# Performance work log

Hardware: AMD Instinct MI355X
Metric: run time of the kernel (lower is better)

The kernel has to match this reference:

```python
import jax, jax.numpy as jnp
import numpy as np

B = 8192      # batch
LAT = 256     # latent_dimension
HID = 512     # hidden_size
INP = 128     # input_size (n_layer_types + 1 feature)
T = 64        # max_length
MLP = 512     # fixed MLP width in source


def _lin(key, fan_in, fan_out):
    kw, kb = jax.random.split(key)
    s = 1.0 / np.sqrt(fan_in)
    W = jax.random.uniform(kw, (fan_in, fan_out), jnp.float32, -s, s)
    b = jax.random.uniform(kb, (fan_out,), jnp.float32, -s, s)
    return W, b


def setup_inputs() -> dict:
    key = jax.random.key(0)
    ks = jax.random.split(key, 16)
    x = jax.random.normal(ks[0], (B, LAT), jnp.float32)
    W1, b1 = _lin(ks[1], LAT, MLP)
    W2, b2 = _lin(ks[2], MLP, MLP)
    W3, b3 = _lin(ks[3], MLP, MLP)
    Wh1, bh1 = _lin(ks[4], MLP, MLP)
    Wh2, bh2 = _lin(ks[5], MLP, HID)
    Wc1, bc1 = _lin(ks[6], MLP, MLP)
    Wc2, bc2 = _lin(ks[7], MLP, HID)
    Wx1, bx1 = _lin(ks[8], MLP, MLP)
    Wx2, bx2 = _lin(ks[9], MLP, INP)
    Wih, bih = _lin(ks[10], INP, 4 * HID)   # LSTM input->gates (i,f,g,o)
    Whh, bhh = _lin(ks[11], HID, 4 * HID)   # LSTM hidden->gates
    Wp, bp = _lin(ks[12], HID, INP)          # predictor head
    return dict(x=x, W1=W1, b1=b1, W2=W2, b2=b2, W3=W3, b3=b3,
                Wh1=Wh1, bh1=bh1, Wh2=Wh2, bh2=bh2,
                Wc1=Wc1, bc1=bc1, Wc2=Wc2, bc2=bc2,
                Wx1=Wx1, bx1=bx1, Wx2=Wx2, bx2=bx2,
                Wih=Wih, bih=bih, Whh=Whh, bhh=bhh, Wp=Wp, bp=bp)


def _lrelu(v):
    return jnp.where(v >= 0, v, 0.2 * v)


def _head(v):
    # split [d-1, 1]: softmax over layer types, sigmoid on feature scalar
    lt = jax.nn.softmax(v[..., :-1], axis=-1)
    ft = jax.nn.sigmoid(v[..., -1:])
    return jnp.concatenate([lt, ft], axis=-1)


def reference(x, W1, b1, W2, b2, W3, b3, Wh1, bh1, Wh2, bh2,
              Wc1, bc1, Wc2, bc2, Wx1, bx1, Wx2, bx2,
              Wih, bih, Whh, bhh, Wp, bp):
    z = _lrelu(x @ W1 + b1)
    z = _lrelu(z @ W2 + b2)
    z = _lrelu(z @ W3 + b3)
    h = _lrelu(z @ Wh1 + bh1) @ Wh2 + bh2          # [B, HID]
    c = _lrelu(z @ Wc1 + bc1) @ Wc2 + bc2          # [B, HID]
    x0 = _head(_lrelu(z @ Wx1 + bx1) @ Wx2 + bx2)  # [B, INP]

    def step(carry, _):
        xt, h, c = carry
        g = xt @ Wih + h @ Whh + (bih + bhh)        # [B, 4*HID]
        i, f, gg, o = jnp.split(g, 4, axis=-1)      # torch gate order i,f,g,o
        c2 = jax.nn.sigmoid(f) * c + jax.nn.sigmoid(i) * jnp.tanh(gg)
        h2 = jax.nn.sigmoid(o) * jnp.tanh(c2)
        nxt = _head(h2 @ Wp + bp)
        return (nxt, h2, c2), nxt

    # The torch loop reruns the LSTM over the growing prefix with the same
    # initial (h,c) and takes the last output; by LSTM causality this equals
    _, ys = jax.lax.scan(step, (x0, h, c), None, length=T)
    return jnp.transpose(ys, (1, 0, 2))  # [B, T, INP]
```

## Files before the change

### kernel.cpp

```cpp
#include <hip/hip_runtime.h>


typedef _Float16 h16;
typedef __attribute__((ext_vector_type(8))) _Float16 f16x8;
typedef __attribute__((ext_vector_type(4))) float f32x4;

#define BB 8192
#define TT 64

__device__ __forceinline__ void gload16(const void* g, void* lds) {
  __builtin_amdgcn_global_load_lds(
      (const __attribute__((address_space(1))) unsigned int*)g,
      (__attribute__((address_space(3))) unsigned int*)lds, 16, 0, 0);
}

__device__ __forceinline__ float sigm(float x) { return 1.f / (1.f + __expf(-x)); }
__device__ __forceinline__ float tanhf_(float x) { return 2.f / (1.f + __expf(-2.f * x)) - 1.f; }

#define RAWBAR()                                           \
  do {                                                     \
    __builtin_amdgcn_s_barrier();                          \
    asm volatile("" ::: "memory");                         \
  } while (0)
#define ENDBAR() RAWBAR()

__global__ __launch_bounds__(512, 4) void gate256x128(
    const h16* __restrict__ A, const h16* __restrict__ Bt,
    const float* __restrict__ bg, float* __restrict__ Cbuf,
    h16* __restrict__ Hout) {
  __shared__ __align__(16) h16 As[3][256 * 32];
  __shared__ __align__(16) h16 Bs[3][128 * 32];
  const int tid = threadIdx.x;
  const int lane = tid & 63;
  const int wid = tid >> 6;
  const int wr = wid >> 1, wc = wid & 1;
  const int m0 = blockIdx.x * 256;
  const int n0 = blockIdx.y * 128;
  const int arow = lane & 15, khi = lane >> 4;

  auto stageTile = [&](int slot, int kt) {
    int gc = (lane & 3) ^ ((lane >> 3) & 3);
    int rl = lane >> 2;
#pragma unroll
    for (int li = 0; li < 2; ++li) {
      int L = li * 8 + wid;
      gload16(A + (size_t)(m0 + L * 16 + rl) * 640 + kt * 32 + gc * 8,
              &As[slot][L * 512]);
    }
    gload16(Bt + (size_t)(n0 + wid * 16 + rl) * 640 + kt * 32 + gc * 8,
            &Bs[slot][wid * 512]);
  };

  f32x4 acc[4][4];
#pragma unroll
  for (int i = 0; i < 4; ++i)
#pragma unroll
    for (int j = 0; j < 4; ++j) acc[i][j] = (f32x4)0.f;
  f16x8 af[4], bf[4];

  auto readAll = [&](int slot) {
#pragma unroll
    for (int q = 0; q < 4; ++q) {
      int rb = wc * 64 + q * 16 + arow;
      bf[q] = *(const f16x8*)&Bs[slot][rb * 32 + (khi ^ ((rb >> 1) & 3)) * 8];
    }
#pragma unroll
    for (int mr = 0; mr < 4; ++mr) {
      int ra = wr * 64 + mr * 16 + arow;
      af[mr] = *(const f16x8*)&As[slot][ra * 32 + (khi ^ ((ra >> 1) & 3)) * 8];
    }
  };
  auto mfmaC = [&]() {
    __builtin_amdgcn_s_setprio(1);
#pragma unroll
    for (int mr = 0; mr < 4; ++mr)
#pragma unroll
      for (int q = 0; q < 4; ++q)
        acc[mr][q] = __builtin_amdgcn_mfma_f32_16x16x32_f16(af[mr], bf[q],
                                                            acc[mr][q], 0, 0, 0);
    __builtin_amdgcn_s_setprio(0);
  };

  stageTile(0, 0);
  stageTile(1, 1);
  stageTile(2, 2);
  asm volatile("s_waitcnt vmcnt(6)" ::: "memory");
  ENDBAR();

  int slot = 0;
#pragma unroll 1
  for (int i = 0; i < 20; ++i) {
    readAll(slot);
    RAWBAR();
    if (i < 17) stageTile(slot, i + 3);
    mfmaC();
    if (i < 17)
      asm volatile("s_waitcnt vmcnt(6)" ::: "memory");
    else if (i == 17)
      asm volatile("s_waitcnt vmcnt(3)" ::: "memory");
    else
      asm volatile("s_waitcnt vmcnt(0)" ::: "memory");
    ENDBAR();
    slot = (slot == 2) ? 0 : slot + 1;
  }

  const int nb = n0 + wc * 64;
  const float bI = bg[nb + arow];
  const float bF = bg[nb + 16 + arow];
  const float bG = bg[nb + 32 + arow];
  const float bO = bg[nb + 48 + arow];
  const int hj = blockIdx.y * 32 + wc * 16 + arow;
#pragma unroll
  for (int mr = 0; mr < 4; ++mr) {
#pragma unroll
    for (int r = 0; r < 4; ++r) {
      int m = m0 + wr * 64 + mr * 16 + khi * 4 + r;
      float gi = sigm(acc[mr][0][r] + bI);
      float gf = sigm(acc[mr][1][r] + bF);
      float gg = tanhf_(acc[mr][2][r] + bG);
      float go = sigm(acc[mr][3][r] + bO);
      size_t ci = (size_t)m * 512 + hj;
      float c2 = gf * Cbuf[ci] + gi * gg;
      Cbuf[ci] = c2;
      Hout[(size_t)m * 640 + 128 + hj] = (h16)(go * tanhf_(c2));
    }
  }
}

__global__ __launch_bounds__(256) void head256(
    const h16* __restrict__ A, int lda, const h16* __restrict__ Bt,
    const float* __restrict__ bias, int nkt, h16* __restrict__ Xout,
    float* __restrict__ ydst, int tstep, int swz) {
  __shared__ __align__(16) h16 As[2][32 * 64];
  __shared__ __align__(16) h16 Bs[2][128 * 64];
  __shared__ float lgs[32 * 132];
  const int tid = threadIdx.x;
  const int lane = tid & 63;
  const int w = tid >> 6;
  const int rs = w & 1, ch = w >> 1;
  const int arow = lane & 15, khi = lane >> 4;
  const int x7 = arow & 7;

  int bid = blockIdx.x;
  int m0;
  if (swz) {
    int g = bid & 7, k = bid >> 3;
    m0 = (g + 8 * (k & 3)) * 256 + (k >> 2) * 32;
  } else {
    m0 = bid * 32;
  }

  auto stageA = [&](int slot, int kt) {
    int rowbase = w * 8;
    int gc = (lane & 7) ^ (lane >> 3);
    int row = rowbase + (lane >> 3);
    gload16(A + (size_t)(m0 + row) * lda + kt * 64 + gc * 8,
            &As[slot][rowbase * 64]);
  };
  auto stageB = [&](int slot, int kt) {
#pragma unroll
    for (int li = 0; li < 4; ++li) {
      int rowbase = li * 32 + w * 8;
      int row = rowbase + (lane >> 3);
      int gc = (lane & 7) ^ (lane >> 3);
      gload16(Bt + (size_t)row * 512 + kt * 64 + gc * 8, &Bs[slot][rowbase * 64]);
    }
  };

  f32x4 acc[4];
#pragma unroll
  for (int j = 0; j < 4; ++j) acc[j] = (f32x4)0.f;

  stageA(0, 0);
  stageB(0, 0);
#pragma unroll 1
  for (int kt = 0; kt < nkt; ++kt) {
    int p = kt & 1;
    if (kt + 1 < nkt) {
      stageA(p ^ 1, kt + 1);
      stageB(p ^ 1, kt + 1);
      asm volatile("s_waitcnt vmcnt(5)" ::: "memory");
    } else {
      asm volatile("s_waitcnt vmcnt(0)" ::: "memory");
    }
    ENDBAR();
#pragma unroll
    for (int kk = 0; kk < 2; ++kk) {
      int kc = kk * 4 + khi;
      int ra = rs * 16 + arow;
      f16x8 afr = *(const f16x8*)&As[p][ra * 64 + (kc ^ x7) * 8];
#pragma unroll
      for (int j = 0; j < 4; ++j) {
        int rb = (ch * 4 + j) * 16 + arow;
        f16x8 bfr = *(const f16x8*)&Bs[p][rb * 64 + (kc ^ x7) * 8];
        acc[j] = __builtin_amdgcn_mfma_f32_16x16x32_f16(afr, bfr, acc[j], 0, 0, 0);
      }
    }
    ENDBAR();
  }

#pragma unroll
  for (int j = 0; j < 4; ++j)
#pragma unroll
    for (int r = 0; r < 4; ++r)
      lgs[(rs * 16 + khi * 4 + r) * 132 + (ch * 4 + j) * 16 + arow] = acc[j][r];
  __syncthreads();
  {
    int row = tid >> 3, g8 = tid & 7;
    float v[16];
    float mx = -1e30f;
#pragma unroll
    for (int q = 0; q < 16; ++q) {
      int col = g8 * 16 + q;
      v[q] = lgs[row * 132 + col] + bias[col];
      if (col != 127) mx = fmaxf(mx, v[q]);
    }
#pragma unroll
    for (int s = 1; s < 8; s <<= 1) mx = fmaxf(mx, __shfl_xor(mx, s, 8));
    float sm = 0.f;
#pragma unroll
    for (int q = 0; q < 16; ++q) {
      int col = g8 * 16 + q;
      if (col != 127) sm += __expf(v[q] - mx);
    }
#pragma unroll
    for (int s = 1; s < 8; s <<= 1) sm += __shfl_xor(sm, s, 8);
    float inv = 1.f / sm;
    h16 xo[16];
    float yo[16];
#pragma unroll
    for (int q = 0; q < 16; ++q) {
      int col = g8 * 16 + q;
      float res = (col == 127) ? sigm(v[q]) : __expf(v[q] - mx) * inv;
      xo[q] = (h16)res;
      yo[q] = res;
    }
    h16* xd = Xout + (size_t)(m0 + row) * 640 + g8 * 16;
    *(f16x8*)xd = *(f16x8*)&xo[0];
    *(f16x8*)(xd + 8) = *(f16x8*)&xo[8];
    if (ydst) {
      float* yd = ydst + ((size_t)(m0 + row) * 64 + tstep) * 128 + g8 * 16;
#pragma unroll
      for (int q = 0; q < 4; ++q) *(f32x4*)(yd + 4 * q) = *(f32x4*)&yo[4 * q];
    }
  }
}

enum { EP_LRELU = 0, EP_LIN16 = 1, EP_F32 = 2 };

template <int EP>
__global__ __launch_bounds__(256) void gemm128(
    const h16* __restrict__ A, int lda, const h16* __restrict__ Bt,
    const float* __restrict__ bias, int K, h16* __restrict__ out16, int ldo,
    int ocol, float* __restrict__ outf, int ldf) {
  __shared__ __align__(16) h16 As[128 * 64];
  __shared__ __align__(16) h16 Bs[128 * 64];
  const int tid = threadIdx.x;
  const int lane = tid & 63;
  const int w = tid >> 6;
  const int m0 = blockIdx.x * 128;
  const int n0 = blockIdx.y * 128;

  f32x4 acc[4][4];
#pragma unroll
  for (int i = 0; i < 4; ++i)
#pragma unroll
    for (int jj = 0; jj < 4; ++jj) acc[i][jj] = (f32x4)0.f;

  const int rh = (w >> 1) * 64;
  const int arow = lane & 15;
  const int khi = lane >> 4;

  const int nkt = K >> 6;
  for (int kt = 0; kt < nkt; ++kt) {
#pragma unroll
    for (int li = 0; li < 4; ++li) {
      int L = w * 4 + li;
      int r = L * 8 + (lane >> 3);
      int c = lane & 7;
      int gc = c ^ (r & 7);
      gload16(A + (size_t)(m0 + r) * lda + kt * 64 + gc * 8, &As[L * 512]);
      gload16(Bt + (size_t)(n0 + r) * K + kt * 64 + gc * 8, &Bs[L * 512]);
    }
    __syncthreads();
#pragma unroll
    for (int kk = 0; kk < 2; ++kk) {
      const int kc = kk * 4 + khi;
      f16x8 af[4], bf[4];
#pragma unroll
      for (int mt = 0; mt < 4; ++mt) {
        int r = rh + mt * 16 + arow;
        af[mt] = *(const f16x8*)&As[r * 64 + (kc ^ (r & 7)) * 8];
      }
#pragma unroll
      for (int jj = 0; jj < 4; ++jj) {
        int nt = (w & 1) * 4 + jj;
        int r = nt * 16 + arow;
        bf[jj] = *(const f16x8*)&Bs[r * 64 + (kc ^ (r & 7)) * 8];
      }
#pragma unroll
      for (int mt = 0; mt < 4; ++mt)
#pragma unroll
        for (int jj = 0; jj < 4; ++jj)
          acc[mt][jj] =
              __builtin_amdgcn_mfma_f32_16x16x32_f16(af[mt], bf[jj], acc[mt][jj], 0, 0, 0);
    }
    __syncthreads();
  }

#pragma unroll
  for (int mt = 0; mt < 4; ++mt) {
#pragma unroll
    for (int jj = 0; jj < 4; ++jj) {
      int nt = (w & 1) * 4 + jj;
      int n = n0 + nt * 16 + arow;
      float bv = bias[n];
#pragma unroll
      for (int r = 0; r < 4; ++r) {
        int m = m0 + rh + mt * 16 + khi * 4 + r;
        float v = acc[mt][jj][r] + bv;
        if constexpr (EP == EP_LRELU) {
          v = v >= 0.f ? v : 0.2f * v;
          out16[(size_t)m * ldo + n] = (h16)v;
        } else if constexpr (EP == EP_LIN16) {
          out16[(size_t)m * ldo + ocol + n] = (h16)v;
        } else {
          outf[(size_t)m * ldf + n] = v;
        }
      }
    }
  }
}

__global__ void cvt16(const float* __restrict__ in, h16* __restrict__ out, int n) {
  int i = blockIdx.x * 256 + threadIdx.x;
  if (i < n) out[i] = (h16)in[i];
}

__global__ void transposeW(const float* __restrict__ W, h16* __restrict__ WT, int K,
                           int N) {
  int i = blockIdx.x * 256 + threadIdx.x;
  if (i >= K * N) return;
  int k = i / N, n = i % N;
  WT[(size_t)n * K + k] = (h16)W[i];
}

__global__ void prep_gate(const float* __restrict__ Wih, const float* __restrict__ Whh,
                          const float* __restrict__ bih, const float* __restrict__ bhh,
                          h16* __restrict__ WgT, float* __restrict__ bg) {
  int i = blockIdx.x * 256 + threadIdx.x;
  if (i >= 2048 * 640) return;
  int np = i / 640, k = i % 640;
  int ny = np >> 7, wcc = (np >> 6) & 1, q = (np >> 4) & 3, jj = np & 15;
  int orig = q * 512 + ny * 32 + wcc * 16 + jj;
  float wv = (k < 128) ? Wih[(size_t)k * 2048 + orig]
                       : Whh[(size_t)(k - 128) * 2048 + orig];
  WgT[i] = (h16)wv;
  if (k == 0) bg[np] = bih[orig] + bhh[orig];
}

extern "C" void kernel_launch(void* const* d_in, const int* in_sizes, int n_in,
                              void* d_out, int out_size, void* d_ws, size_t ws_size,
                              hipStream_t stream) {
  const float* x = (const float*)d_in[0];
  const float* W1 = (const float*)d_in[1];
  const float* b1 = (const float*)d_in[2];
  const float* W2 = (const float*)d_in[3];
  const float* b2 = (const float*)d_in[4];
  const float* W3 = (const float*)d_in[5];
  const float* b3 = (const float*)d_in[6];
  const float* Wh1 = (const float*)d_in[7];
  const float* bh1 = (const float*)d_in[8];
  const float* Wh2 = (const float*)d_in[9];
  const float* bh2 = (const float*)d_in[10];
  const float* Wc1 = (const float*)d_in[11];
  const float* bc1 = (const float*)d_in[12];
  const float* Wc2 = (const float*)d_in[13];
  const float* bc2 = (const float*)d_in[14];
  const float* Wx1 = (const float*)d_in[15];
  const float* bx1 = (const float*)d_in[16];
  const float* Wx2 = (const float*)d_in[17];
  const float* bx2 = (const float*)d_in[18];
  const float* Wih = (const float*)d_in[19];
  const float* bih = (const float*)d_in[20];
  const float* Whh = (const float*)d_in[21];
  const float* bhh = (const float*)d_in[22];
  const float* Wp = (const float*)d_in[23];
  const float* bp = (const float*)d_in[24];

  char* ws = (char*)d_ws;
  size_t off = 0;
  auto take = [&](size_t bytes) -> void* {
    void* p = ws + off;
    off += (bytes + 255) & ~(size_t)255;
    return p;
  };
  h16* X16 = (h16*)take((size_t)BB * 256 * 2);
  h16* Za = (h16*)take((size_t)BB * 512 * 2);
  h16* Zb = (h16*)take((size_t)BB * 512 * 2);
  h16* XHa = (h16*)take((size_t)BB * 640 * 2);
  h16* XHb = (h16*)take((size_t)BB * 640 * 2);
  float* C = (float*)take((size_t)BB * 512 * 4);
  h16* W1T = (h16*)take(256 * 512 * 2);
  h16* W2T = (h16*)take(512 * 512 * 2);
  h16* W3T = (h16*)take(512 * 512 * 2);
  h16* Wh1T = (h16*)take(512 * 512 * 2);
  h16* Wh2T = (h16*)take(512 * 512 * 2);
  h16* Wc1T = (h16*)take(512 * 512 * 2);
  h16* Wc2T = (h16*)take(512 * 512 * 2);
  h16* Wx1T = (h16*)take(512 * 512 * 2);
  h16* Wx2T = (h16*)take(128 * 512 * 2);
  h16* WpT = (h16*)take(128 * 512 * 2);
  h16* WgT = (h16*)take((size_t)2048 * 640 * 2);
  float* bg = (float*)take(2048 * 4);

  dim3 blk(256);
  cvt16<<<(BB * 256 + 255) / 256, blk, 0, stream>>>(x, X16, BB * 256);
  transposeW<<<(256 * 512 + 255) / 256, blk, 0, stream>>>(W1, W1T, 256, 512);
  transposeW<<<(512 * 512 + 255) / 256, blk, 0, stream>>>(W2, W2T, 512, 512);
  transposeW<<<(512 * 512 + 255) / 256, blk, 0, stream>>>(W3, W3T, 512, 512);
  transposeW<<<(512 * 512 + 255) / 256, blk, 0, stream>>>(Wh1, Wh1T, 512, 512);
  transposeW<<<(512 * 512 + 255) / 256, blk, 0, stream>>>(Wh2, Wh2T, 512, 512);
  transposeW<<<(512 * 512 + 255) / 256, blk, 0, stream>>>(Wc1, Wc1T, 512, 512);
  transposeW<<<(512 * 512 + 255) / 256, blk, 0, stream>>>(Wc2, Wc2T, 512, 512);
  transposeW<<<(512 * 512 + 255) / 256, blk, 0, stream>>>(Wx1, Wx1T, 512, 512);
  transposeW<<<(512 * 128 + 255) / 256, blk, 0, stream>>>(Wx2, Wx2T, 512, 128);
  transposeW<<<(512 * 128 + 255) / 256, blk, 0, stream>>>(Wp, WpT, 512, 128);
  prep_gate<<<(2048 * 640 + 255) / 256, blk, 0, stream>>>(Wih, Whh, bih, bhh, WgT, bg);

  gemm128<EP_LRELU><<<dim3(64, 4), blk, 0, stream>>>(X16, 256, W1T, b1, 256, Za, 512, 0, nullptr, 0);
  gemm128<EP_LRELU><<<dim3(64, 4), blk, 0, stream>>>(Za, 512, W2T, b2, 512, Zb, 512, 0, nullptr, 0);
  gemm128<EP_LRELU><<<dim3(64, 4), blk, 0, stream>>>(Zb, 512, W3T, b3, 512, Za, 512, 0, nullptr, 0);
  gemm128<EP_LRELU><<<dim3(64, 4), blk, 0, stream>>>(Za, 512, Wh1T, bh1, 512, Zb, 512, 0, nullptr, 0);
  gemm128<EP_LIN16><<<dim3(64, 4), blk, 0, stream>>>(Zb, 512, Wh2T, bh2, 512, XHa, 640, 128, nullptr, 0);
  gemm128<EP_LRELU><<<dim3(64, 4), blk, 0, stream>>>(Za, 512, Wc1T, bc1, 512, Zb, 512, 0, nullptr, 0);
  gemm128<EP_F32><<<dim3(64, 4), blk, 0, stream>>>(Zb, 512, Wc2T, bc2, 512, nullptr, 0, 0, C, 512);
  gemm128<EP_LRELU><<<dim3(64, 4), blk, 0, stream>>>(Za, 512, Wx1T, bx1, 512, Zb, 512, 0, nullptr, 0);
  head256<<<256, blk, 0, stream>>>(Zb, 512, Wx2T, bx2, 8, XHa, nullptr, 0, 0);

  float* yout = (float*)d_out;
  for (int t = 0; t < TT; ++t) {
    h16* in_ = (t & 1) ? XHb : XHa;
    h16* out_ = (t & 1) ? XHa : XHb;
    gate256x128<<<dim3(32, 16), dim3(512), 0, stream>>>(in_, WgT, bg, C, out_);
    head256<<<256, blk, 0, stream>>>(out_ + 128, 640, WpT, bp, 8, out_, yout, t, 1);
  }
}
```

Before: 2.800 ms.

## Enlarge LSTM gate GEMM tile to 256x256 with four-stage LDS ring

```diff
diff --git a/kernel.cpp b/kernel.cpp
--- a/kernel.cpp
+++ b/kernel.cpp
@@ -17,25 +17,24 @@
 __device__ __forceinline__ float sigm(float x) { return 1.f / (1.f + __expf(-x)); }
 __device__ __forceinline__ float tanhf_(float x) { return 2.f / (1.f + __expf(-2.f * x)) - 1.f; }
 
-#define RAWBAR()                                           \
+#define ENDBAR()                                           \
   do {                                                     \
     __builtin_amdgcn_s_barrier();                          \
     asm volatile("" ::: "memory");                         \
   } while (0)
-#define ENDBAR() RAWBAR()
-
-__global__ __launch_bounds__(512, 4) void gate256x128(
+
+__global__ __launch_bounds__(512, 2) void gate32x4(
     const h16* __restrict__ A, const h16* __restrict__ Bt,
     const float* __restrict__ bg, float* __restrict__ Cbuf,
     h16* __restrict__ Hout) {
-  __shared__ __align__(16) h16 As[3][256 * 32];
-  __shared__ __align__(16) h16 Bs[3][128 * 32];
+  __shared__ __align__(16) h16 As[4][256 * 32];
+  __shared__ __align__(16) h16 Bs[4][256 * 32];
   const int tid = threadIdx.x;
   const int lane = tid & 63;
   const int wid = tid >> 6;
-  const int wr = wid >> 1, wc = wid & 1;
+  const int wr = wid >> 2, wc = wid & 3;
   const int m0 = blockIdx.x * 256;
-  const int n0 = blockIdx.y * 128;
+  const int n0 = blockIdx.y * 256;
   const int arow = lane & 15, khi = lane >> 4;
 
   auto stageTile = [&](int slot, int kt) {
@@ -47,16 +46,20 @@
       gload16(A + (size_t)(m0 + L * 16 + rl) * 640 + kt * 32 + gc * 8,
               &As[slot][L * 512]);
     }
-    gload16(Bt + (size_t)(n0 + wid * 16 + rl) * 640 + kt * 32 + gc * 8,
-            &Bs[slot][wid * 512]);
-  };
-
-  f32x4 acc[4][4];
-#pragma unroll
-  for (int i = 0; i < 4; ++i)
+#pragma unroll
+    for (int li = 0; li < 2; ++li) {
+      int L = li * 8 + wid;
+      gload16(Bt + (size_t)(n0 + L * 16 + rl) * 640 + kt * 32 + gc * 8,
+              &Bs[slot][L * 512]);
+    }
+  };
+
+  f32x4 acc[8][4];
+#pragma unroll
+  for (int i = 0; i < 8; ++i)
 #pragma unroll
     for (int j = 0; j < 4; ++j) acc[i][j] = (f32x4)0.f;
-  f16x8 af[4], bf[4];
+  f16x8 af[8], bf[4];
 
   auto readAll = [&](int slot) {
 #pragma unroll
@@ -65,15 +68,15 @@
       bf[q] = *(const f16x8*)&Bs[slot][rb * 32 + (khi ^ ((rb >> 1) & 3)) * 8];
     }
 #pragma unroll
-    for (int mr = 0; mr < 4; ++mr) {
-      int ra = wr * 64 + mr * 16 + arow;
+    for (int mr = 0; mr < 8; ++mr) {
+      int ra = wr * 128 + mr * 16 + arow;
       af[mr] = *(const f16x8*)&As[slot][ra * 32 + (khi ^ ((ra >> 1) & 3)) * 8];
     }
   };
   auto mfmaC = [&]() {
     __builtin_amdgcn_s_setprio(1);
 #pragma unroll
-    for (int mr = 0; mr < 4; ++mr)
+    for (int mr = 0; mr < 8; ++mr)
 #pragma unroll
       for (int q = 0; q < 4; ++q)
         acc[mr][q] = __builtin_amdgcn_mfma_f32_16x16x32_f16(af[mr], bf[q],
@@ -84,24 +87,25 @@
   stageTile(0, 0);
   stageTile(1, 1);
   stageTile(2, 2);
-  asm volatile("s_waitcnt vmcnt(6)" ::: "memory");
+  asm volatile("s_waitcnt vmcnt(8)" ::: "memory");
   ENDBAR();
 
-  int slot = 0;
 #pragma unroll 1
-  for (int i = 0; i < 20; ++i) {
-    readAll(slot);
-    RAWBAR();
-    if (i < 17) stageTile(slot, i + 3);
-    mfmaC();
-    if (i < 17)
-      asm volatile("s_waitcnt vmcnt(6)" ::: "memory");
-    else if (i == 17)
-      asm volatile("s_waitcnt vmcnt(3)" ::: "memory");
-    else
-      asm volatile("s_waitcnt vmcnt(0)" ::: "memory");
-    ENDBAR();
-    slot = (slot == 2) ? 0 : slot + 1;
+  for (int ii = 0; ii < 5; ++ii) {
+#pragma unroll
+    for (int p = 0; p < 4; ++p) {
+      const int t = 4 * ii + p;
+      readAll(p);
+      if (t < 17) stageTile((p + 3) & 3, t + 3);
+      mfmaC();
+      if (t < 17)
+        asm volatile("s_waitcnt vmcnt(8)" ::: "memory");
+      else if (t == 17)
+        asm volatile("s_waitcnt vmcnt(4)" ::: "memory");
+      else if (t == 18)
+        asm volatile("s_waitcnt vmcnt(0)" ::: "memory");
+      ENDBAR();
+    }
   }
 
   const int nb = n0 + wc * 64;
@@ -109,16 +113,16 @@
   const float bF = bg[nb + 16 + arow];
   const float bG = bg[nb + 32 + arow];
   const float bO = bg[nb + 48 + arow];
-  const int hj = blockIdx.y * 32 + wc * 16 + arow;
-#pragma unroll
-  for (int mr = 0; mr < 4; ++mr) {
+  const int hj = blockIdx.y * 64 + wc * 16 + arow;
+#pragma unroll
+  for (int mrep = 0; mrep < 8; ++mrep) {
 #pragma unroll
     for (int r = 0; r < 4; ++r) {
-      int m = m0 + wr * 64 + mr * 16 + khi * 4 + r;
-      float gi = sigm(acc[mr][0][r] + bI);
-      float gf = sigm(acc[mr][1][r] + bF);
-      float gg = tanhf_(acc[mr][2][r] + bG);
-      float go = sigm(acc[mr][3][r] + bO);
+      int m = m0 + wr * 128 + mrep * 16 + khi * 4 + r;
+      float gi = sigm(acc[mrep][0][r] + bI);
+      float gf = sigm(acc[mrep][1][r] + bF);
+      float gg = tanhf_(acc[mrep][2][r] + bG);
+      float go = sigm(acc[mrep][3][r] + bO);
       size_t ci = (size_t)m * 512 + hj;
       float c2 = gf * Cbuf[ci] + gi * gg;
       Cbuf[ci] = c2;
@@ -351,8 +355,8 @@
   int i = blockIdx.x * 256 + threadIdx.x;
   if (i >= 2048 * 640) return;
   int np = i / 640, k = i % 640;
-  int ny = np >> 7, wcc = (np >> 6) & 1, q = (np >> 4) & 3, jj = np & 15;
-  int orig = q * 512 + ny * 32 + wcc * 16 + jj;
+  int by = np >> 8, wcc = (np >> 6) & 3, q = (np >> 4) & 3, jj = np & 15;
+  int orig = q * 512 + by * 64 + wcc * 16 + jj;
   float wv = (k < 128) ? Wih[(size_t)k * 2048 + orig]
                        : Whh[(size_t)(k - 128) * 2048 + orig];
   WgT[i] = (h16)wv;
@@ -442,7 +446,7 @@
   for (int t = 0; t < TT; ++t) {
     h16* in_ = (t & 1) ? XHb : XHa;
     h16* out_ = (t & 1) ? XHa : XHb;
-    gate256x128<<<dim3(32, 16), dim3(512), 0, stream>>>(in_, WgT, bg, C, out_);
+    gate32x4<<<dim3(32, 8), dim3(512), 0, stream>>>(in_, WgT, bg, C, out_);
     head256<<<256, blk, 0, stream>>>(out_ + 128, 640, WpT, bp, 8, out_, yout, t, 1);
   }
 }
```

Result: no change. 2.828 ms (+1.0%).
